# Performance work log

Hardware: AMD Instinct MI355X
Metric: run time of the kernel (lower is better)

## Reference

```python
import jax, jax.numpy as jnp
import numpy as np

KS = 2            # kernel_size
NUM_SHARED = 3    # len(num_shared_channels)
NBR_PARAM = 3     # nbr_param_layers
COUT = 128        # num_shared_channels[-1] == num_inputs
NUM_INPUTS = 128
D_R = 320         # ts2vec_output_dims
GEN_LEN = NBR_PARAM * COUT * COUT * KS


def _causal_conv(x, w, b, d):
    # x: [N, Ci, T], w: [Co, Ci, K], b: [Co]; left-pad (K-1)*d == pad+chomp in torch
    N, Ci, T = x.shape
    K = w.shape[-1]
    pad = (K - 1) * d
    xp = jnp.pad(x, ((0, 0), (0, 0), (pad, 0)))
    out = jnp.zeros((N, w.shape[0], T), dtype=x.dtype)
    for k in range(K):  # K==2, tiny static loop
        out = out + jnp.einsum('oc,nct->not', w[:, :, k], xp[:, :, k * d:k * d + T])
    return out + b[None, :, None]


def _causal_conv_group(x, w, d):
    # groups=N conv with per-sample weights. x: [N, C, T], w: [N, Co, C, K], no bias
    N, C, T = x.shape
    K = w.shape[-1]
    pad = (K - 1) * d
    xp = jnp.pad(x, ((0, 0), (0, 0), (pad, 0)))
    out = jnp.zeros((N, w.shape[1], T), dtype=x.dtype)
    for k in range(K):
        out = out + jnp.einsum('noc,nct->not', w[..., k], xp[:, :, k * d:k * d + T])
    return out


def setup_inputs() -> dict:
    key = jax.random.key(0)
    ks = jax.random.split(key, 12)
    N, T = 16, 1024
    x = jax.random.normal(ks[0], (N, T, NUM_INPUTS), dtype=jnp.float32)
    r = jax.random.normal(ks[1], (N, D_R), dtype=jnp.float32)
    # shared TemporalBlock params (in==out==COUT, so no downsample conv)
    wscale = 1.0 / np.sqrt(COUT * KS)
    shared_w1 = wscale * jax.random.normal(ks[2], (NUM_SHARED, COUT, COUT, KS), dtype=jnp.float32)
    shared_b1 = 0.01 * jax.random.normal(ks[3], (NUM_SHARED, COUT), dtype=jnp.float32)
    shared_w2 = wscale * jax.random.normal(ks[4], (NUM_SHARED, COUT, COUT, KS), dtype=jnp.float32)
    shared_b2 = 0.01 * jax.random.normal(ks[5], (NUM_SHARED, COUT), dtype=jnp.float32)
    # hypernetwork (f_param_generator) + additive base weights (last_conv_layers)
    fparam_W = 0.01 * jax.random.normal(ks[6], (GEN_LEN, D_R), dtype=jnp.float32)
    fparam_b = 0.01 * jax.random.normal(ks[7], (GEN_LEN,), dtype=jnp.float32)
    last_bias = 0.001 * jax.random.normal(ks[8], (GEN_LEN,), dtype=jnp.float32) + 1.0 / (KS * COUT)
    # output head
    lin_W = (1.0 / np.sqrt(COUT)) * jax.random.normal(ks[9], (NUM_INPUTS, COUT), dtype=jnp.float32)
    lin_b = 0.01 * jax.random.normal(ks[10], (NUM_INPUTS,), dtype=jnp.float32)
    return {"x": x, "r": r, "f_out_same_in_size": 1,
            "shared_w1": shared_w1, "shared_b1": shared_b1,
            "shared_w2": shared_w2, "shared_b2": shared_b2,
            "fparam_W": fparam_W, "fparam_b": fparam_b, "last_bias": last_bias,
            "lin_W": lin_W, "lin_b": lin_b}


def reference(x, r, f_out_same_in_size, shared_w1, shared_b1, shared_w2, shared_b2,
              fparam_W, fparam_b, last_bias, lin_W, lin_b):
    N, T, _ = x.shape
    h = jnp.swapaxes(x, 1, 2)  # [N, C, T]
    # shared TemporalBlocks (dropout p=0 -> identity)
    for i in range(NUM_SHARED):
        d = 2 ** i
        res = h
        a = jax.nn.relu(_causal_conv(h, shared_w1[i], shared_b1[i], d))
        a = jax.nn.relu(_causal_conv(a, shared_w2[i], shared_b2[i], d))
        h = jax.nn.relu(a + res)
    # hypernet-generated per-sample grouped conv layers
    gen = r @ fparam_W.T + fparam_b + last_bias           # [N, GEN_LEN]
    allw = gen.reshape(NBR_PARAM, N, COUT, COUT, KS)      # same layout as torch .view
    for i in range(NBR_PARAM):
        d = 2 ** (NUM_SHARED + i)
        res = h
        c = _causal_conv_group(h, allw[i], d)
        h = jax.nn.relu(jax.nn.relu(c) + res)             # relu(dropout(relu(c)) + res), p=0
    out = jnp.einsum('nct,oc->nto', h, lin_W) + lin_b     # [N, T, NUM_INPUTS]
    if not f_out_same_in_size:
        out = out[:, -1, :]
    return out
```

## Files before the change

kernel.cpp:

```cpp
#include <hip/hip_runtime.h>

#define NB    16
#define TLEN  1024
#define CCH   128
#define DR    320

typedef _Float16 h8 __attribute__((ext_vector_type(8)));
typedef _Float16 h4 __attribute__((ext_vector_type(4)));
typedef _Float16 h2 __attribute__((ext_vector_type(2)));
typedef float    f4 __attribute__((ext_vector_type(4)));

__device__ __forceinline__ void gload16h(const _Float16* g, _Float16* l) {
  __builtin_amdgcn_global_load_lds(
      (const __attribute__((address_space(1))) void*)g,
      (__attribute__((address_space(3))) void*)l, 16, 0, 0);
}
__device__ __forceinline__ void gload16f(const float* g, float* l) {
  __builtin_amdgcn_global_load_lds(
      (const __attribute__((address_space(1))) void*)g,
      (__attribute__((address_space(3))) void*)l, 16, 0, 0);
}

__global__ __launch_bounds__(256) void k_init(const float* __restrict__ x,
                                              const float* __restrict__ w1,
                                              const float* __restrict__ w2,
                                              const float* __restrict__ linw,
                                              const float* __restrict__ fb,
                                              const float* __restrict__ lb,
                                              _Float16* __restrict__ h0,
                                              _Float16* __restrict__ Wsh,
                                              _Float16* __restrict__ linWh,
                                              float* __restrict__ fblb2) {
  int i = blockIdx.x * 256 + threadIdx.x;
  const float4* src = (const float4*)x + (size_t)i * 2;
  float4 a = src[0], b = src[1];
  h8 v;
  v[0] = (_Float16)a.x; v[1] = (_Float16)a.y; v[2] = (_Float16)a.z; v[3] = (_Float16)a.w;
  v[4] = (_Float16)b.x; v[5] = (_Float16)b.y; v[6] = (_Float16)b.z; v[7] = (_Float16)b.w;
  *(h8*)(h0 + (size_t)i * 8) = v;

  if (i < 6 * 32768) {
    int c = i & 127, k = (i >> 7) & 1, o = (i >> 8) & 127, i3 = i >> 15;
    const float* srcw = (i3 < 3) ? (w1 + i3 * 32768) : (w2 + (i3 - 3) * 32768);
    Wsh[i] = (_Float16)srcw[(o * 128 + c) * 2 + k];
  }
  if (i < 16384) linWh[i] = (_Float16)linw[i];
  if (i < 98304) fblb2[i] = fb[i] + lb[i];
}

struct SGen {
  float buf[3][32 * DR];
  float csc[4][16][16];
  float fbl[512];
};
struct SPair {
  _Float16 hin[84 * 128];
  _Float16 a[80 * 128];
};
union alignas(16) SU { SGen g; SPair p; };

__device__ __forceinline__ void gen_body(SGen& S, int bid, int tid,
                                         const float* __restrict__ r,
                                         const float* __restrict__ fW,
                                         const float* __restrict__ fblb2,
                                         _Float16* __restrict__ wg) {
  constexpr int NT = 16;
  const size_t rbase = (size_t)bid * 512;

  const int l = tid & 63, w = tid >> 6;
  const int l15 = l & 15, lh = l >> 4;
  const int rt = w >> 1, kh = w & 1;

  f4 rx[5], ry[5];
  const float* rp = r + l15 * DR + kh * 160 + lh * 8;
#pragma unroll
  for (int cb = 0; cb < 5; cb++) {
    rx[cb] = *(const f4*)(rp + cb * 32);
    ry[cb] = *(const f4*)(rp + cb * 32 + 4);
  }
  if (tid < 128) gload16f(fblb2 + rbase + tid * 4, S.fbl + tid * 4);
#pragma unroll
  for (int t = 0; t < 3; t++) {
    const float* s = fW + (rbase + (size_t)t * 32) * DR;
#pragma unroll
    for (int i = 0; i < 10; i++) {
      int f = tid + i * 256;
      gload16f(s + (size_t)f * 4, (float*)S.buf[t] + (size_t)f * 4);
    }
  }
  h8 bfr[5];
#pragma unroll
  for (int cb = 0; cb < 5; cb++) {
    h8 v;
    v[0] = (_Float16)rx[cb][0]; v[1] = (_Float16)rx[cb][1];
    v[2] = (_Float16)rx[cb][2]; v[3] = (_Float16)rx[cb][3];
    v[4] = (_Float16)ry[cb][0]; v[5] = (_Float16)ry[cb][1];
    v[6] = (_Float16)ry[cb][2]; v[7] = (_Float16)ry[cb][3];
    bfr[cb] = v;
  }
  asm volatile("s_waitcnt vmcnt(20) lgkmcnt(0)" ::: "memory");
  __builtin_amdgcn_s_barrier();
  __builtin_amdgcn_sched_barrier(0);

  const int rn = tid >> 4, rk = (tid >> 3) & 1, rcq = tid & 7;

  for (int j = 0; j < NT; j++) {
    const float* bp = (const float*)S.buf[j % 3];
    f4 acc = {0.f, 0.f, 0.f, 0.f};
    const float* arow = bp + (rt * 16 + l15) * DR + kh * 160 + lh * 8;
#pragma unroll
    for (int cb = 0; cb < 5; cb++) {
      f4 x = *(const f4*)(arow + cb * 32);
      f4 y = *(const f4*)(arow + cb * 32 + 4);
      h8 a;
      a[0] = (_Float16)x[0]; a[1] = (_Float16)x[1];
      a[2] = (_Float16)x[2]; a[3] = (_Float16)x[3];
      a[4] = (_Float16)y[0]; a[5] = (_Float16)y[1];
      a[6] = (_Float16)y[2]; a[7] = (_Float16)y[3];
      acc = __builtin_amdgcn_mfma_f32_16x16x32_f16(a, bfr[cb], acc, 0, 0, 0);
    }
#pragma unroll
    for (int rr = 0; rr < 4; rr++) S.csc[w][lh * 4 + rr][l15] = acc[rr];

    asm volatile("s_waitcnt lgkmcnt(0)" ::: "memory");
    __builtin_amdgcn_s_barrier();
    __builtin_amdgcn_sched_barrier(0);

    {
      const unsigned g32 = (unsigned)(rbase + (size_t)j * 32);
      const unsigned G = g32 >> 15, o = (g32 >> 8) & 127u, c0 = (g32 & 255u) >> 1;
      h2 v2;
#pragma unroll
      for (int i = 0; i < 2; i++) {
        int rl32 = (rcq * 2 + i) * 2 + rk;
        int hp = (rl32 >> 4) * 2, rr2 = rl32 & 15;
        float s = S.csc[hp][rr2][rn] + S.csc[hp + 1][rr2][rn] + S.fbl[j * 32 + rl32];
        v2[i] = (_Float16)s;
      }
      unsigned q = 3u * (unsigned)rn + G;
      *(h2*)&wg[(((size_t)q * 128 + o) * 2 + rk) * 128 + c0 + rcq * 2] = v2;
    }
    __builtin_amdgcn_sched_barrier(0);

    if (j + 3 < NT) {
      float* dstb = (float*)S.buf[j % 3];
      const float* src = fW + (rbase + (size_t)(j + 3) * 32) * DR;
#pragma unroll
      for (int i = 0; i < 10; i++) {
        int f = tid + i * 256;
        gload16f(src + (size_t)f * 4, dstb + (size_t)f * 4);
      }
    }

    if (j + 4 <= NT)
      asm volatile("s_waitcnt vmcnt(20) lgkmcnt(0)" ::: "memory");
    else if (j + 3 == NT)
      asm volatile("s_waitcnt vmcnt(10) lgkmcnt(0)" ::: "memory");
    else
      asm volatile("s_waitcnt vmcnt(0) lgkmcnt(0)" ::: "memory");
    __builtin_amdgcn_s_barrier();
    __builtin_amdgcn_sched_barrier(0);
  }
}

template <int D>
__device__ __forceinline__ void pair_body(SPair& S, int tx, int n, int tid,
                                          const _Float16* in, _Float16* out,
                                          const _Float16* w1p, const _Float16* w2p,
                                          const float* b1p, const float* b2p) {
  constexpr int HA = 16;
  constexpr int HI = HA + D;
  constexpr int RIN = 80 + D;
  static_assert(RIN * 128 <= sizeof(SPair::hin) / sizeof(_Float16), "hin size");
  _Float16* hin_l = S.hin;
  _Float16* a_l = S.a;
  const int t0 = tx * 64;
  const _Float16* inN = in + (size_t)n * (TLEN * CCH);

  if (tx == 0) {
    for (int f = tid; f < HI * 16; f += 256)
      *(int4*)(hin_l + (size_t)f * 8) = make_int4(0, 0, 0, 0);
    for (int f = HI * 16 + tid; f < RIN * 16; f += 256) {
      int p = f >> 4, l16 = f & 15;
      int c8 = (l16 ^ (p & 15)) << 3;
      gload16h(inN + (t0 - HI + p) * 128 + c8, hin_l + f * 8);
    }
  } else {
    for (int f = tid; f < RIN * 16; f += 256) {
      int p = f >> 4, l16 = f & 15;
      int c8 = (l16 ^ (p & 15)) << 3;
      gload16h(inN + (t0 - HI + p) * 128 + c8, hin_l + f * 8);
    }
  }
  __syncthreads();

  const int l = tid & 63, w = tid >> 6;
  const int l15 = l & 15, lh = l >> 4;
  const int o0 = w * 32;

  f4 acc1[2][5] = {};
#pragma unroll
  for (int tap = 0; tap < 2; tap++) {
#pragma unroll
    for (int cb = 0; cb < 4; cb++) {
      const int c0 = cb * 32 + lh * 8;
      h8 a[2], bfr[5];
#pragma unroll
      for (int i2 = 0; i2 < 2; i2++) {
        int o = o0 + i2 * 16 + l15;
        a[i2] = *(const h8*)&w1p[(o * 2 + tap) * 128 + c0];
      }
#pragma unroll
      for (int jt = 0; jt < 5; jt++) {
        int p = jt * 16 + l15 + tap * D;
        int cs = c0 ^ ((p & 15) << 3);
        bfr[jt] = *(const h8*)&hin_l[p * 128 + cs];
      }
#pragma unroll
      for (int i2 = 0; i2 < 2; i2++)
#pragma unroll
        for (int jt = 0; jt < 5; jt++)
          acc1[i2][jt] = __builtin_amdgcn_mfma_f32_16x16x32_f16(
              a[i2], bfr[jt], acc1[i2][jt], 0, 0, 0);
    }
  }
#pragma unroll
  for (int i2 = 0; i2 < 2; i2++) {
    f4 bv = *(const f4*)&b1p[o0 + i2 * 16 + lh * 4];
    const int base8 = o0 + i2 * 16 + (lh >> 1) * 8;
    const int sub = (lh & 1) * 4;
#pragma unroll
    for (int jt = 0; jt < 5; jt++) {
      int p = jt * 16 + l15;
      h4 sv;
      if (tx == 0 && jt == 0) {
        sv[0] = sv[1] = sv[2] = sv[3] = (_Float16)0.f;
      } else {
        f4 v = acc1[i2][jt];
#pragma unroll
        for (int rr = 0; rr < 4; rr++) sv[rr] = (_Float16)fmaxf(v[rr] + bv[rr], 0.f);
      }
      *(h4*)&a_l[p * 128 + (base8 ^ ((p & 15) << 3)) + sub] = sv;
    }
  }
  __syncthreads();

  f4 acc2[2][4] = {};
#pragma unroll
  for (int tap = 0; tap < 2; tap++) {
#pragma unroll
    for (int cb = 0; cb < 4; cb++) {
      const int c0 = cb * 32 + lh * 8;
      h8 a[2], bfr[4];
#pragma unroll
      for (int i2 = 0; i2 < 2; i2++) {
        int o = o0 + i2 * 16 + l15;
        a[i2] = *(const h8*)&w2p[(o * 2 + tap) * 128 + c0];
      }
#pragma unroll
      for (int jt = 0; jt < 4; jt++) {
        int pa = jt * 16 + l15 + (HA - D) + tap * D;
        int cs = c0 ^ ((pa & 15) << 3);
        bfr[jt] = *(const h8*)&a_l[pa * 128 + cs];
      }
#pragma unroll
      for (int i2 = 0; i2 < 2; i2++)
#pragma unroll
        for (int jt = 0; jt < 4; jt++)
          acc2[i2][jt] = __builtin_amdgcn_mfma_f32_16x16x32_f16(
              a[i2], bfr[jt], acc2[i2][jt], 0, 0, 0);
    }
  }

  _Float16* outN = out + (size_t)n * (TLEN * CCH);
#pragma unroll
  for (int i2 = 0; i2 < 2; i2++) {
    f4 bv = *(const f4*)&b2p[o0 + i2 * 16 + lh * 4];
    const int base8 = o0 + i2 * 16 + (lh >> 1) * 8;
    const int sub = (lh & 1) * 4;
#pragma unroll
    for (int jt = 0; jt < 4; jt++) {
      int t = t0 + jt * 16 + l15;
      int pr = jt * 16 + l15 + HA + D;
      h4 rv = *(const h4*)&hin_l[pr * 128 + (base8 ^ ((pr & 15) << 3)) + sub];
      f4 v = acc2[i2][jt];
      h4 sv;
#pragma unroll
      for (int rr = 0; rr < 4; rr++) {
        float z = fmaxf(v[rr] + bv[rr], 0.f);
        sv[rr] = (_Float16)fmaxf(z + (float)rv[rr], 0.f);
      }
      *(h4*)&outN[t * 128 + o0 + i2 * 16 + lh * 4] = sv;
    }
  }
}

__global__ __launch_bounds__(256, 1) void k_genpair(
    const float* __restrict__ r, const float* __restrict__ fW,
    const float* __restrict__ fblb2, _Float16* __restrict__ wg,
    const _Float16* __restrict__ h0, _Float16* __restrict__ h1,
    const _Float16* __restrict__ Wsh,
    const float* __restrict__ b1, const float* __restrict__ b2) {
  __shared__ SU su;
  const int bid = blockIdx.x, tid = threadIdx.x;
  if (bid < 192) {
    gen_body(su.g, bid, tid, r, fW, fblb2, wg);
  } else {
    int q = bid - 192;
    pair_body<1>(su.p, q & 15, q >> 4, tid, h0, h1,
                 Wsh, Wsh + 3 * 32768, b1, b2);
  }
}

template <int D>
__global__ __launch_bounds__(256) void k_pair(const _Float16* __restrict__ in,
                                              _Float16* __restrict__ out,
                                              const _Float16* __restrict__ w1p,
                                              const _Float16* __restrict__ w2p,
                                              const float* __restrict__ b1p,
                                              const float* __restrict__ b2p) {
  __shared__ SPair sp;
  pair_body<D>(sp, blockIdx.x, blockIdx.y, threadIdx.x, in, out, w1p, w2p,
               b1p, b2p);
}

template <int D, int NJ>
__device__ __forceinline__ void gstage(const _Float16* __restrict__ Wl,
                                       const _Float16* __restrict__ inb,
                                       _Float16* __restrict__ outb,
                                       int zlim, int tid) {
  const int l = tid & 63, w = tid >> 6;
  const int l15 = l & 15, lh = l >> 4;
  const int o0 = w * 32;
  f4 acc[2][NJ] = {};

#pragma unroll
  for (int tap = 0; tap < 2; tap++) {
#pragma unroll
    for (int cb = 0; cb < 4; cb++) {
      const int c0 = cb * 32 + 8 * lh;
      h8 a[2], bfr[NJ];
#pragma unroll
      for (int i2 = 0; i2 < 2; i2++) {
        int o = o0 + i2 * 16 + l15;
        int cs = c0 ^ ((o & 15) << 3);
        a[i2] = *(const h8*)&Wl[(o * 2 + tap) * 128 + cs];
      }
#pragma unroll
      for (int jt = 0; jt < NJ; jt++) {
        int p = jt * 16 + l15 + tap * D;
        int cs = c0 ^ ((p & 15) << 3);
        bfr[jt] = *(const h8*)&inb[p * 128 + cs];
      }
#pragma unroll
      for (int i2 = 0; i2 < 2; i2++)
#pragma unroll
        for (int jt = 0; jt < NJ; jt++)
          acc[i2][jt] = __builtin_amdgcn_mfma_f32_16x16x32_f16(
              a[i2], bfr[jt], acc[i2][jt], 0, 0, 0);
    }
  }

#pragma unroll
  for (int i2 = 0; i2 < 2; i2++) {
    const int base8 = o0 + i2 * 16 + (lh >> 1) * 8;
    const int sub = (lh & 1) * 4;
#pragma unroll
    for (int jt = 0; jt < NJ; jt++) {
      int rrow = jt * 16 + l15;
      int pr = rrow + D;
      h4 sv;
      if (rrow < zlim) {
        sv[0] = sv[1] = sv[2] = sv[3] = (_Float16)0.f;
      } else {
        h4 rv = *(const h4*)&inb[pr * 128 + (base8 ^ ((pr & 15) << 3)) + sub];
        f4 v = acc[i2][jt];
#pragma unroll
        for (int rr = 0; rr < 4; rr++) {
          float z = fmaxf(v[rr], 0.f);
          sv[rr] = (_Float16)fmaxf(z + (float)rv[rr], 0.f);
        }
      }
      *(h4*)&outb[rrow * 128 + (base8 ^ (l15 << 3)) + sub] = sv;
    }
  }
}

__global__ __launch_bounds__(256, 1) void k_group(const _Float16* __restrict__ in,
                                                  float* __restrict__ outp,
                                                  const _Float16* __restrict__ wg,
                                                  const _Float16* __restrict__ linWh,
                                                  const float* __restrict__ lbias) {
  __shared__ _Float16 bufA[120 * 128];
  __shared__ _Float16 bufB[112 * 128];
  __shared__ _Float16 Wl[256 * 128];
  const int tid = threadIdx.x;
  const int tx = blockIdx.x, n = blockIdx.y;
  const int t0 = tx * 64;
  const _Float16* inN = in + (size_t)n * (TLEN * CCH);
  const _Float16* wp1 = wg + (size_t)n * 32768;
  const _Float16* wp2 = wg + 524288 + (size_t)n * 32768;
  const _Float16* wp3 = wg + 1048576 + (size_t)n * 32768;

  if (tx == 0) {
    for (int f = tid; f < 56 * 16; f += 256)
      *(int4*)(bufA + (size_t)f * 8) = make_int4(0, 0, 0, 0);
    for (int f = 56 * 16 + tid; f < 120 * 16; f += 256) {
      int p = f >> 4, l16 = f & 15;
      int c8 = (l16 ^ (p & 15)) << 3;
      gload16h(inN + (t0 - 56 + p) * 128 + c8, bufA + f * 8);
    }
  } else {
    for (int f = tid; f < 120 * 16; f += 256) {
      int p = f >> 4, l16 = f & 15;
      int c8 = (l16 ^ (p & 15)) << 3;
      gload16h(inN + (t0 - 56 + p) * 128 + c8, bufA + f * 8);
    }
  }
  for (int f = tid; f < 4096; f += 256) {
    int row = f >> 4, l16 = f & 15;
    int c8 = (l16 ^ ((row >> 1) & 15)) << 3;
    gload16h(wp1 + row * 128 + c8, Wl + f * 8);
  }
  __syncthreads();

  gstage<8, 7>(Wl, bufA, bufB, (tx == 0) ? 48 : 0, tid);
  __syncthreads();
  for (int f = tid; f < 4096; f += 256) {
    int row = f >> 4, l16 = f & 15;
    int c8 = (l16 ^ ((row >> 1) & 15)) << 3;
    gload16h(wp2 + row * 128 + c8, Wl + f * 8);
  }
  __syncthreads();

  gstage<16, 6>(Wl, bufB, bufA, (tx == 0) ? 32 : 0, tid);
  __syncthreads();
  for (int f = tid; f < 4096; f += 256) {
    int row = f >> 4, l16 = f & 15;
    int c8 = (l16 ^ ((row >> 1) & 15)) << 3;
    gload16h(wp3 + row * 128 + c8, Wl + f * 8);
  }
  __syncthreads();

  gstage<32, 4>(Wl, bufA, bufB, 0, tid);
  __syncthreads();

  const int l = tid & 63, w = tid >> 6;
  const int l15 = l & 15, lh = l >> 4;
  const int o0 = w * 32;
  f4 acc3[2][4] = {};
#pragma unroll
  for (int cb = 0; cb < 4; cb++) {
    const int c0 = cb * 32 + lh * 8;
    h8 a[2], bfr[4];
#pragma unroll
    for (int i2 = 0; i2 < 2; i2++) {
      int o = o0 + i2 * 16 + l15;
      a[i2] = *(const h8*)&linWh[o * 128 + c0];
    }
#pragma unroll
    for (int jt = 0; jt < 4; jt++) {
      int p = jt * 16 + l15;
      int cs = c0 ^ ((p & 15) << 3);
      bfr[jt] = *(const h8*)&bufB[p * 128 + cs];
    }
#pragma unroll
    for (int i2 = 0; i2 < 2; i2++)
#pragma unroll
      for (int jt = 0; jt < 4; jt++)
        acc3[i2][jt] = __builtin_amdgcn_mfma_f32_16x16x32_f16(
            a[i2], bfr[jt], acc3[i2][jt], 0, 0, 0);
  }

#pragma unroll
  for (int i2 = 0; i2 < 2; i2++) {
    int o = o0 + i2 * 16 + lh * 4;
    f4 bv = *(const f4*)&lbias[o];
#pragma unroll
    for (int jt = 0; jt < 4; jt++) {
      int t = t0 + jt * 16 + l15;
      f4 v = acc3[i2][jt];
      float4 sv = make_float4(v[0] + bv[0], v[1] + bv[1], v[2] + bv[2], v[3] + bv[3]);
      *(float4*)&outp[((size_t)n * TLEN + t) * CCH + o] = sv;
    }
  }
}

extern "C" void kernel_launch(void* const* d_in, const int* in_sizes, int n_in,
                              void* d_out, int out_size, void* d_ws, size_t ws_size,
                              hipStream_t stream) {
  const float* x  = (const float*)d_in[0];
  const float* r  = (const float*)d_in[1];
  const float* w1 = (const float*)d_in[3];
  const float* b1 = (const float*)d_in[4];
  const float* w2 = (const float*)d_in[5];
  const float* b2 = (const float*)d_in[6];
  const float* fW = (const float*)d_in[7];
  const float* fb = (const float*)d_in[8];
  const float* lb = (const float*)d_in[9];
  const float* lw = (const float*)d_in[10];
  const float* lbias = (const float*)d_in[11];
  float* out = (float*)d_out;

  _Float16* h0    = (_Float16*)d_ws;
  _Float16* h1    = h0 + 2097152;
  _Float16* Wsh   = h1 + 2097152;
  _Float16* linWh = Wsh + 393216;
  _Float16* Wg    = linWh + 16384;
  float*    fblb2 = (float*)(Wg + 1572864);

  k_init<<<1024, 256, 0, stream>>>(x, w1, w2, lw, fb, lb, h0, Wsh, linWh, fblb2);
  k_genpair<<<448, 256, 0, stream>>>(r, fW, fblb2, Wg, h0, h1, Wsh, b1, b2);

  const dim3 cg(16, 16);
  k_pair<2><<<cg, 256, 0, stream>>>(h1, h0, Wsh + 1 * 32768, Wsh + 4 * 32768,
                                    b1 + 128, b2 + 128);
  k_pair<4><<<cg, 256, 0, stream>>>(h0, h1, Wsh + 2 * 32768, Wsh + 5 * 32768,
                                    b1 + 256, b2 + 256);
  k_group<<<cg, 256, 0, stream>>>(h1, out, Wg, linWh, lbias);
}
```

Measured before the change: 75.34 us.

## Fuse all three shared temporal blocks into one kernel with halo recompute

The three shared TemporalBlock pair kernels are merged into one fused per-tile pipeline inside k_genpair. Each tile loads a 48-step halo once and runs all three dilations back to back in LDS. The intermediate activations no longer round-trip through global memory, and two kernel launches are removed. In exchange the halo convolutions are recomputed, the grid shrinks to 64 pair blocks each looping over 4 tiles alongside the 192 gen blocks, and the larger LDS footprint may lower occupancy.

```diff
diff --git a/kernel.cpp b/kernel.cpp
--- a/kernel.cpp
+++ b/kernel.cpp
@@ -53,11 +53,12 @@
   float csc[4][16][16];
   float fbl[512];
 };
-struct SPair {
-  _Float16 hin[84 * 128];
-  _Float16 a[80 * 128];
+struct SPairC {
+  _Float16 B0[128 * 128];
+  _Float16 B1[128 * 128];
+  _Float16 B2[112 * 128];
 };
-union alignas(16) SU { SGen g; SPair p; };
+union alignas(16) SU { SGen g; SPairC p; };
 
 __device__ __forceinline__ void gen_body(SGen& S, int bid, int tid,
                                          const float* __restrict__ r,
@@ -163,63 +164,45 @@
   }
 }
 
-template <int D>
-__device__ __forceinline__ void pair_body(SPair& S, int tx, int n, int tid,
-                                          const _Float16* in, _Float16* out,
-                                          const _Float16* w1p, const _Float16* w2p,
-                                          const float* b1p, const float* b2p) {
-  constexpr int HA = 16;
-  constexpr int HI = HA + D;
-  constexpr int RIN = 80 + D;
-  static_assert(RIN * 128 <= sizeof(SPair::hin) / sizeof(_Float16), "hin size");
-  _Float16* hin_l = S.hin;
-  _Float16* a_l = S.a;
-  const int t0 = tx * 64;
-  const _Float16* inN = in + (size_t)n * (TLEN * CCH);
-
-  if (tx == 0) {
-    for (int f = tid; f < HI * 16; f += 256)
-      *(int4*)(hin_l + (size_t)f * 8) = make_int4(0, 0, 0, 0);
-    for (int f = HI * 16 + tid; f < RIN * 16; f += 256) {
-      int p = f >> 4, l16 = f & 15;
-      int c8 = (l16 ^ (p & 15)) << 3;
-      gload16h(inN + (t0 - HI + p) * 128 + c8, hin_l + f * 8);
-    }
-  } else {
-    for (int f = tid; f < RIN * 16; f += 256) {
-      int p = f >> 4, l16 = f & 15;
-      int c8 = (l16 ^ (p & 15)) << 3;
-      gload16h(inN + (t0 - HI + p) * 128 + c8, hin_l + f * 8);
-    }
-  }
-  __syncthreads();
-
+template <int D, int NJ, bool GOUT>
+__device__ __forceinline__ void pstage(const _Float16* __restrict__ w1p,
+                                       const _Float16* __restrict__ w2p,
+                                       const float* __restrict__ b1p,
+                                       const float* __restrict__ b2p,
+                                       const _Float16* __restrict__ inb,
+                                       _Float16* __restrict__ ab,
+                                       _Float16* __restrict__ outb,
+                                       _Float16* __restrict__ goutN, int t0,
+                                       int zlimA, int zlimO, int tid) {
+  constexpr int NA = NJ + 1;
   const int l = tid & 63, w = tid >> 6;
   const int l15 = l & 15, lh = l >> 4;
   const int o0 = w * 32;
-
-  f4 acc1[2][5] = {};
+  const int base8 = o0 + (lh >> 1) * 8;
+  const int sub = (lh & 1) * 4;
+
+  f4 acc1[2][NA] = {};
 #pragma unroll
   for (int tap = 0; tap < 2; tap++) {
 #pragma unroll
     for (int cb = 0; cb < 4; cb++) {
       const int c0 = cb * 32 + lh * 8;
-      h8 a[2], bfr[5];
+      h8 a[2], bfr[NA];
 #pragma unroll
       for (int i2 = 0; i2 < 2; i2++) {
         int o = o0 + i2 * 16 + l15;
         a[i2] = *(const h8*)&w1p[(o * 2 + tap) * 128 + c0];
       }
 #pragma unroll
-      for (int jt = 0; jt < 5; jt++) {
+      for (int jt = 0; jt < NA; jt++) {
         int p = jt * 16 + l15 + tap * D;
         int cs = c0 ^ ((p & 15) << 3);
-        bfr[jt] = *(const h8*)&hin_l[p * 128 + cs];
+        bfr[jt] = *(const h8*)&inb[p * 128 + cs];
       }
 #pragma unroll
       for (int i2 = 0; i2 < 2; i2++)
 #pragma unroll
-        for (int jt = 0; jt < 5; jt++)
+        for (int jt = 0; jt < NA; jt++)
           acc1[i2][jt] = __builtin_amdgcn_mfma_f32_16x16x32_f16(
               a[i2], bfr[jt], acc1[i2][jt], 0, 0, 0);
     }
@@ -227,70 +210,75 @@
 #pragma unroll
   for (int i2 = 0; i2 < 2; i2++) {
     f4 bv = *(const f4*)&b1p[o0 + i2 * 16 + lh * 4];
-    const int base8 = o0 + i2 * 16 + (lh >> 1) * 8;
-    const int sub = (lh & 1) * 4;
-#pragma unroll
-    for (int jt = 0; jt < 5; jt++) {
-      int p = jt * 16 + l15;
+    const int b8 = base8 + i2 * 16;
+#pragma unroll
+    for (int jt = 0; jt < NA; jt++) {
+      int q = jt * 16 + l15;
       h4 sv;
-      if (tx == 0 && jt == 0) {
+      if (q < zlimA) {
         sv[0] = sv[1] = sv[2] = sv[3] = (_Float16)0.f;
       } else {
         f4 v = acc1[i2][jt];
 #pragma unroll
         for (int rr = 0; rr < 4; rr++) sv[rr] = (_Float16)fmaxf(v[rr] + bv[rr], 0.f);
       }
-      *(h4*)&a_l[p * 128 + (base8 ^ ((p & 15) << 3)) + sub] = sv;
-    }
-  }
-  __syncthreads();
-
-  f4 acc2[2][4] = {};
+      *(h4*)&ab[q * 128 + (b8 ^ ((q & 15) << 3)) + sub] = sv;
+    }
+  }
+  __syncthreads();
+
+  f4 acc2[2][NJ] = {};
 #pragma unroll
   for (int tap = 0; tap < 2; tap++) {
 #pragma unroll
     for (int cb = 0; cb < 4; cb++) {
       const int c0 = cb * 32 + lh * 8;
-      h8 a[2], bfr[4];
+      h8 a[2], bfr[NJ];
 #pragma unroll
       for (int i2 = 0; i2 < 2; i2++) {
         int o = o0 + i2 * 16 + l15;
         a[i2] = *(const h8*)&w2p[(o * 2 + tap) * 128 + c0];
       }
 #pragma unroll
-      for (int jt = 0; jt < 4; jt++) {
-        int pa = jt * 16 + l15 + (HA - D) + tap * D;
+      for (int jt = 0; jt < NJ; jt++) {
+        int pa = jt * 16 + l15 + (16 - 2 * D) + tap * D;
         int cs = c0 ^ ((pa & 15) << 3);
-        bfr[jt] = *(const h8*)&a_l[pa * 128 + cs];
+        bfr[jt] = *(const h8*)&ab[pa * 128 + cs];
       }
 #pragma unroll
       for (int i2 = 0; i2 < 2; i2++)
 #pragma unroll
-        for (int jt = 0; jt < 4; jt++)
+        for (int jt = 0; jt < NJ; jt++)
           acc2[i2][jt] = __builtin_amdgcn_mfma_f32_16x16x32_f16(
               a[i2], bfr[jt], acc2[i2][jt], 0, 0, 0);
     }
   }
-
-  _Float16* outN = out + (size_t)n * (TLEN * CCH);
 #pragma unroll
   for (int i2 = 0; i2 < 2; i2++) {
     f4 bv = *(const f4*)&b2p[o0 + i2 * 16 + lh * 4];
-    const int base8 = o0 + i2 * 16 + (lh >> 1) * 8;
-    const int sub = (lh & 1) * 4;
-#pragma unroll
-    for (int jt = 0; jt < 4; jt++) {
-      int t = t0 + jt * 16 + l15;
-      int pr = jt * 16 + l15 + HA + D;
-      h4 rv = *(const h4*)&hin_l[pr * 128 + (base8 ^ ((pr & 15) << 3)) + sub];
-      f4 v = acc2[i2][jt];
+    const int b8 = base8 + i2 * 16;
+#pragma unroll
+    for (int jt = 0; jt < NJ; jt++) {
+      int r = jt * 16 + l15;
+      int pr = r + 16;
       h4 sv;
-#pragma unroll
-      for (int rr = 0; rr < 4; rr++) {
-        float z = fmaxf(v[rr] + bv[rr], 0.f);
-        sv[rr] = (_Float16)fmaxf(z + (float)rv[rr], 0.f);
-      }
-      *(h4*)&outN[t * 128 + o0 + i2 * 16 + lh * 4] = sv;
+      if (r < zlimO) {
+        sv[0] = sv[1] = sv[2] = sv[3] = (_Float16)0.f;
+      } else {
+        h4 rv = *(const h4*)&inb[pr * 128 + (b8 ^ ((pr & 15) << 3)) + sub];
+        f4 v = acc2[i2][jt];
+#pragma unroll
+        for (int rr = 0; rr < 4; rr++) {
+          float z = fmaxf(v[rr] + bv[rr], 0.f);
+          sv[rr] = (_Float16)fmaxf(z + (float)rv[rr], 0.f);
+        }
+      }
+      if (GOUT) {
+        int t = t0 + r;
+        *(h4*)&goutN[t * 128 + o0 + i2 * 16 + lh * 4] = sv;
+      } else {
+        *(h4*)&outb[r * 128 + (b8 ^ (l15 << 3)) + sub] = sv;
+      }
     }
   }
 }
@@ -305,23 +293,46 @@
   const int bid = blockIdx.x, tid = threadIdx.x;
   if (bid < 192) {
     gen_body(su.g, bid, tid, r, fW, fblb2, wg);
-  } else {
-    int q = bid - 192;
-    pair_body<1>(su.p, q & 15, q >> 4, tid, h0, h1,
-                 Wsh, Wsh + 3 * 32768, b1, b2);
-  }
-}
-
-template <int D>
-__global__ __launch_bounds__(256) void k_pair(const _Float16* __restrict__ in,
-                                              _Float16* __restrict__ out,
-                                              const _Float16* __restrict__ w1p,
-                                              const _Float16* __restrict__ w2p,
-                                              const float* __restrict__ b1p,
-                                              const float* __restrict__ b2p) {
-  __shared__ SPair sp;
-  pair_body<D>(sp, blockIdx.x, blockIdx.y, threadIdx.x, in, out, w1p, w2p,
-               b1p, b2p);
+    return;
+  }
+  const int pb = bid - 192;
+  for (int rep = 0; rep < 4; rep++) {
+    const int q = pb + rep * 64;
+    const int tx = q & 15, n = q >> 4;
+    const int t0 = tx * 64;
+    const _Float16* inN = h0 + (size_t)n * (TLEN * CCH);
+    __syncthreads();
+
+    if (tx == 0) {
+      for (int f = tid; f < 48 * 16; f += 256)
+        *(int4*)(su.p.B0 + (size_t)f * 8) = make_int4(0, 0, 0, 0);
+      for (int f = 48 * 16 + tid; f < 112 * 16; f += 256) {
+        int p = f >> 4, l16 = f & 15;
+        int c8 = (l16 ^ (p & 15)) << 3;
+        gload16h(inN + (t0 - 48 + p) * 128 + c8, su.p.B0 + f * 8);
+      }
+    } else {
+      for (int f = tid; f < 112 * 16; f += 256) {
+        int p = f >> 4, l16 = f & 15;
+        int c8 = (l16 ^ (p & 15)) << 3;
+        gload16h(inN + (t0 - 48 + p) * 128 + c8, su.p.B0 + f * 8);
+      }
+    }
+    __syncthreads();
+
+    pstage<1, 6, false>(Wsh, Wsh + 3 * 32768, b1, b2,
+                        su.p.B0, su.p.B1, su.p.B2, nullptr, t0,
+                        (tx == 0) ? 47 : 0, (tx == 0) ? 32 : 0, tid);
+    __syncthreads();
+    pstage<2, 5, false>(Wsh + 1 * 32768, Wsh + 4 * 32768, b1 + 128, b2 + 128,
+                        su.p.B2, su.p.B1, su.p.B0, nullptr, t0,
+                        (tx == 0) ? 30 : 0, (tx == 0) ? 16 : 0, tid);
+    __syncthreads();
+    pstage<4, 4, true>(Wsh + 2 * 32768, Wsh + 5 * 32768, b1 + 256, b2 + 256,
+                       su.p.B0, su.p.B2, nullptr,
+                       h1 + (size_t)n * (TLEN * CCH), t0,
+                       (tx == 0) ? 12 : 0, 0, tid);
+  }
 }
 
 template <int D, int NJ>
@@ -510,12 +521,6 @@
   float*    fblb2 = (float*)(Wg + 1572864);
 
   k_init<<<1024, 256, 0, stream>>>(x, w1, w2, lw, fb, lb, h0, Wsh, linWh, fblb2);
-  k_genpair<<<448, 256, 0, stream>>>(r, fW, fblb2, Wg, h0, h1, Wsh, b1, b2);
-
-  const dim3 cg(16, 16);
-  k_pair<2><<<cg, 256, 0, stream>>>(h1, h0, Wsh + 1 * 32768, Wsh + 4 * 32768,
-                                    b1 + 128, b2 + 128);
-  k_pair<4><<<cg, 256, 0, stream>>>(h0, h1, Wsh + 2 * 32768, Wsh + 5 * 32768,
-                                    b1 + 256, b2 + 256);
-  k_group<<<cg, 256, 0, stream>>>(h1, out, Wg, linWh, lbias);
-}
+  k_genpair<<<256, 256, 0, stream>>>(r, fW, fblb2, Wg, h0, h1, Wsh, b1, b2);
+  k_group<<<dim3(16, 16), 256, 0, stream>>>(h1, out, Wg, linWh, lbias);
+}
```

Result: slower. 123.8 us (+64.4%).

## Fuse dilation-2 and dilation-4 temporal blocks into one kernel with halo recompute

Applied to the files above, without the earlier changes.

Replaces the two separate k_pair launches for the second and third shared temporal blocks with a single kernel. Each block loads a 96-row input window with halo into LDS, computes both convs of block two, and keeps that output in LDS as input to block three. Only the final result is written to global memory. This removes one launch and one full intermediate round trip through global memory, at the cost of recomputing overlapping halo rows and using more LDS per block, which may lower occupancy.

```diff
diff --git a/kernel.cpp b/kernel.cpp
--- a/kernel.cpp
+++ b/kernel.cpp
@@ -312,16 +312,168 @@
   }
 }
 
-template <int D>
-__global__ __launch_bounds__(256) void k_pair(const _Float16* __restrict__ in,
-                                              _Float16* __restrict__ out,
-                                              const _Float16* __restrict__ w1p,
-                                              const _Float16* __restrict__ w2p,
-                                              const float* __restrict__ b1p,
-                                              const float* __restrict__ b2p) {
-  __shared__ SPair sp;
-  pair_body<D>(sp, blockIdx.x, blockIdx.y, threadIdx.x, in, out, w1p, w2p,
-               b1p, b2p);
+template <int D, int NJ, bool GOUT>
+__device__ __forceinline__ void pstage(const _Float16* __restrict__ w1p,
+                                       const _Float16* __restrict__ w2p,
+                                       const float* __restrict__ b1p,
+                                       const float* __restrict__ b2p,
+                                       const _Float16* __restrict__ inb,
+                                       _Float16* __restrict__ ab,
+                                       _Float16* __restrict__ outb,
+                                       _Float16* __restrict__ goutN, int t0,
+                                       int zlimA, int zlimO, int tid) {
+  constexpr int NA = NJ + 1;
+  const int l = tid & 63, w = tid >> 6;
+  const int l15 = l & 15, lh = l >> 4;
+  const int o0 = w * 32;
+  const int base8 = o0 + (lh >> 1) * 8;
+  const int sub = (lh & 1) * 4;
+
+  f4 acc1[2][NA] = {};
+#pragma unroll
+  for (int tap = 0; tap < 2; tap++) {
+#pragma unroll
+    for (int cb = 0; cb < 4; cb++) {
+      const int c0 = cb * 32 + lh * 8;
+      h8 a[2], bfr[NA];
+#pragma unroll
+      for (int i2 = 0; i2 < 2; i2++) {
+        int o = o0 + i2 * 16 + l15;
+        a[i2] = *(const h8*)&w1p[(o * 2 + tap) * 128 + c0];
+      }
+#pragma unroll
+      for (int jt = 0; jt < NA; jt++) {
+        int p = jt * 16 + l15 + tap * D;
+        int cs = c0 ^ ((p & 15) << 3);
+        bfr[jt] = *(const h8*)&inb[p * 128 + cs];
+      }
+#pragma unroll
+      for (int i2 = 0; i2 < 2; i2++)
+#pragma unroll
+        for (int jt = 0; jt < NA; jt++)
+          acc1[i2][jt] = __builtin_amdgcn_mfma_f32_16x16x32_f16(
+              a[i2], bfr[jt], acc1[i2][jt], 0, 0, 0);
+    }
+  }
+#pragma unroll
+  for (int i2 = 0; i2 < 2; i2++) {
+    f4 bv = *(const f4*)&b1p[o0 + i2 * 16 + lh * 4];
+    const int b8 = base8 + i2 * 16;
+#pragma unroll
+    for (int jt = 0; jt < NA; jt++) {
+      int q = jt * 16 + l15;
+      h4 sv;
+      if (q < zlimA) {
+        sv[0] = sv[1] = sv[2] = sv[3] = (_Float16)0.f;
+      } else {
+        f4 v = acc1[i2][jt];
+#pragma unroll
+        for (int rr = 0; rr < 4; rr++) sv[rr] = (_Float16)fmaxf(v[rr] + bv[rr], 0.f);
+      }
+      *(h4*)&ab[q * 128 + (b8 ^ ((q & 15) << 3)) + sub] = sv;
+    }
+  }
+  __syncthreads();
+
+  f4 acc2[2][NJ] = {};
+#pragma unroll
+  for (int tap = 0; tap < 2; tap++) {
+#pragma unroll
+    for (int cb = 0; cb < 4; cb++) {
+      const int c0 = cb * 32 + lh * 8;
+      h8 a[2], bfr[NJ];
+#pragma unroll
+      for (int i2 = 0; i2 < 2; i2++) {
+        int o = o0 + i2 * 16 + l15;
+        a[i2] = *(const h8*)&w2p[(o * 2 + tap) * 128 + c0];
+      }
+#pragma unroll
+      for (int jt = 0; jt < NJ; jt++) {
+        int pa = jt * 16 + l15 + (16 - 2 * D) + tap * D;
+        int cs = c0 ^ ((pa & 15) << 3);
+        bfr[jt] = *(const h8*)&ab[pa * 128 + cs];
+      }
+#pragma unroll
+      for (int i2 = 0; i2 < 2; i2++)
+#pragma unroll
+        for (int jt = 0; jt < NJ; jt++)
+          acc2[i2][jt] = __builtin_amdgcn_mfma_f32_16x16x32_f16(
+              a[i2], bfr[jt], acc2[i2][jt], 0, 0, 0);
+    }
+  }
+#pragma unroll
+  for (int i2 = 0; i2 < 2; i2++) {
+    f4 bv = *(const f4*)&b2p[o0 + i2 * 16 + lh * 4];
+    const int b8 = base8 + i2 * 16;
+#pragma unroll
+    for (int jt = 0; jt < NJ; jt++) {
+      int r = jt * 16 + l15;
+      int pr = r + 16;
+      h4 sv;
+      if (r < zlimO) {
+        sv[0] = sv[1] = sv[2] = sv[3] = (_Float16)0.f;
+      } else {
+        h4 rv = *(const h4*)&inb[pr * 128 + (b8 ^ ((pr & 15) << 3)) + sub];
+        f4 v = acc2[i2][jt];
+#pragma unroll
+        for (int rr = 0; rr < 4; rr++) {
+          float z = fmaxf(v[rr] + bv[rr], 0.f);
+          sv[rr] = (_Float16)fmaxf(z + (float)rv[rr], 0.f);
+        }
+      }
+      if (GOUT) {
+        int t = t0 + r;
+        *(h4*)&goutN[t * 128 + o0 + i2 * 16 + lh * 4] = sv;
+      } else {
+        *(h4*)&outb[r * 128 + (b8 ^ (l15 << 3)) + sub] = sv;
+      }
+    }
+  }
+}
+
+__global__ __launch_bounds__(256) void k_pair24(const _Float16* __restrict__ in,
+                                                _Float16* __restrict__ out,
+                                                const _Float16* __restrict__ Wsh,
+                                                const float* __restrict__ b1,
+                                                const float* __restrict__ b2) {
+  __shared__ _Float16 B0[104 * 128];
+  __shared__ _Float16 B1[96 * 128];
+  __shared__ _Float16 B2[88 * 128];
+  const int tid = threadIdx.x;
+  const int tx = blockIdx.x, n = blockIdx.y;
+  const int t0 = tx * 64;
+  const _Float16* inN = in + (size_t)n * (TLEN * CCH);
+
+  for (int f = 96 * 16 + tid; f < 104 * 16; f += 256)
+    *(int4*)(B0 + (size_t)f * 8) = make_int4(0, 0, 0, 0);
+  for (int f = 80 * 16 + tid; f < 88 * 16; f += 256)
+    *(int4*)(B2 + (size_t)f * 8) = make_int4(0, 0, 0, 0);
+
+  if (tx == 0) {
+    for (int f = tid; f < 32 * 16; f += 256)
+      *(int4*)(B0 + (size_t)f * 8) = make_int4(0, 0, 0, 0);
+    for (int f = 32 * 16 + tid; f < 96 * 16; f += 256) {
+      int p = f >> 4, l16 = f & 15;
+      int c8 = (l16 ^ (p & 15)) << 3;
+      gload16h(inN + (t0 - 32 + p) * 128 + c8, B0 + f * 8);
+    }
+  } else {
+    for (int f = tid; f < 96 * 16; f += 256) {
+      int p = f >> 4, l16 = f & 15;
+      int c8 = (l16 ^ (p & 15)) << 3;
+      gload16h(inN + (t0 - 32 + p) * 128 + c8, B0 + f * 8);
+    }
+  }
+  __syncthreads();
+
+  pstage<2, 5, false>(Wsh + 1 * 32768, Wsh + 4 * 32768, b1 + 128, b2 + 128,
+                      B0, B1, B2, nullptr, t0,
+                      (tx == 0) ? 30 : 0, (tx == 0) ? 16 : 0, tid);
+  __syncthreads();
+  pstage<4, 4, true>(Wsh + 2 * 32768, Wsh + 5 * 32768, b1 + 256, b2 + 256,
+                     B2, B1, nullptr,
+                     out + (size_t)n * (TLEN * CCH), t0,
+                     (tx == 0) ? 12 : 0, 0, tid);
 }
 
 template <int D, int NJ>
@@ -511,11 +663,6 @@
 
   k_init<<<1024, 256, 0, stream>>>(x, w1, w2, lw, fb, lb, h0, Wsh, linWh, fblb2);
   k_genpair<<<448, 256, 0, stream>>>(r, fW, fblb2, Wg, h0, h1, Wsh, b1, b2);
-
-  const dim3 cg(16, 16);
-  k_pair<2><<<cg, 256, 0, stream>>>(h1, h0, Wsh + 1 * 32768, Wsh + 4 * 32768,
-                                    b1 + 128, b2 + 128);
-  k_pair<4><<<cg, 256, 0, stream>>>(h0, h1, Wsh + 2 * 32768, Wsh + 5 * 32768,
-                                    b1 + 256, b2 + 256);
-  k_group<<<cg, 256, 0, stream>>>(h1, out, Wg, linWh, lbias);
-}
+  k_pair24<<<dim3(16, 16), 256, 0, stream>>>(h1, h0, Wsh, b1, b2);
+  k_group<<<dim3(16, 16), 256, 0, stream>>>(h0, out, Wg, linWh, lbias);
+}
```

Result: faster. 72.78 us (-3.4%).
